# Kernel optimization log

Hardware: AMD Instinct MI355X
Metric: run time of the kernel (lower is better)

The kernel has to match this reference:

```python
import jax, jax.numpy as jnp
import numpy as np

D = 1024  # inputSize = stateSize = hiddenSize

def _linear_params(key, fan_in, fan_out):
    k1, k2 = jax.random.split(key)
    lim = 1.0 / np.sqrt(fan_in)
    W = jax.random.uniform(k1, (fan_out, fan_in), jnp.float32, -lim, lim)
    b = jax.random.uniform(k2, (fan_out,), jnp.float32, -lim, lim)
    return W, b

def setup_inputs() -> dict:
    key = jax.random.key(0)
    ks = jax.random.split(key, 6)
    x = jax.random.normal(ks[0], (64, D, 200), dtype=jnp.float32)
    W_in, b_in = _linear_params(ks[1], D, D)      # l1_in
    W_hid, b_hid = _linear_params(ks[2], D, D)    # l1_hid
    W2, b2 = _linear_params(ks[3], D, D)          # l2
    W3, b3 = _linear_params(ks[4], D, D)          # l3
    W_out, b_out = _linear_params(ks[5], D, D)    # l_out
    etas = jnp.full((5,), 0.01, dtype=jnp.float32)
    return {"x": x, "W_in": W_in, "b_in": b_in, "W_hid": W_hid, "b_hid": b_hid,
            "W2": W2, "b2": b2, "W3": W3, "b3": b3,
            "W_out": W_out, "b_out": b_out, "etas": etas}

def reference(x, W_in, b_in, W_hid, b_hid, W2, b2, W3, b3, W_out, b_out, etas):
    B = x.shape[0]
    elu = jax.nn.elu

    def step(h0, x_t):  # x_t: [B, D]
        wx = x_t @ W_in.T + b_in
        h = h0
        for k in range(5):  # five fixed-point iterations (eta1..eta5)
            u = (h + h0) @ W_hid.T + b_hid
            F1 = elu(u + wx)
            Fn = elu(elu(F1 @ W2.T + b2) @ W3.T + b3)
            h = h + etas[k] * (Fn - (h + h0))
        y = h @ W_out.T + b_out
        return h, y

    h0 = jnp.zeros((B, x.shape[1]), dtype=x.dtype)
    xs = jnp.transpose(x, (2, 0, 1))  # [T, B, D]
    _, ys = jax.lax.scan(step, h0, xs)  # ys: [T, B, D]
    return jnp.transpose(ys, (1, 2, 0))  # [B, D, T]
```

## Files before the change

### kernel.cpp

```cpp
#include <hip/hip_runtime.h>
#include <cmath>

#define DD 1024
#define TT 200
#define NWG 256
#define THR 512

__device__ __forceinline__ float eluf(float x) { return x > 0.f ? x : expm1f(x); }

__global__ __launch_bounds__(256) void transpose_k(const float* __restrict__ src,
                                                   float* __restrict__ dst) {
  __shared__ float tile[32][33];
  const int bx = blockIdx.x << 5;
  const int by = blockIdx.y << 5;
  const int tx = threadIdx.x & 31;
  const int ty = threadIdx.x >> 5;
#pragma unroll
  for (int i = 0; i < 4; ++i) {
    int r = ty + (i << 3);
    tile[r][tx] = src[(size_t)(bx + r) * DD + by + tx];
  }
  __syncthreads();
#pragma unroll
  for (int i = 0; i < 4; ++i) {
    int r = ty + (i << 3);
    dst[(size_t)(by + r) * DD + bx + tx] = tile[tx][r];
  }
}

__global__ __launch_bounds__(256) void wx_kernel(const float* __restrict__ x,
                                                 const float* __restrict__ Win,
                                                 const float* __restrict__ bin,
                                                 float* __restrict__ wxT) {
  const int gw = (blockIdx.x << 2) | (threadIdx.x >> 6);
  const int lane = threadIdx.x & 63;
  const int noct = gw & 127;
  const int tt = (gw >> 7) & 3;
  const int b = gw >> 9;
  const int n0 = noct << 3;
  const int t = (tt << 6) + lane;
  const int tl = t < TT ? t : (TT - 1);
  const float* xp = x + (size_t)b * DD * TT + tl;
  float acc[8];
#pragma unroll
  for (int j = 0; j < 8; ++j) acc[j] = 0.f;
  for (int k = 0; k < DD; k += 4) {
    float x0 = xp[(size_t)(k + 0) * TT];
    float x1 = xp[(size_t)(k + 1) * TT];
    float x2 = xp[(size_t)(k + 2) * TT];
    float x3 = xp[(size_t)(k + 3) * TT];
#pragma unroll
    for (int j = 0; j < 8; ++j) {
      const float4 w = *(const float4*)(Win + (size_t)(n0 + j) * DD + k);
      acc[j] = fmaf(x0, w.x, fmaf(x1, w.y, fmaf(x2, w.z, fmaf(x3, w.w, acc[j]))));
    }
  }
  if (t < TT) {
#pragma unroll
    for (int j = 0; j < 8; ++j)
      wxT[((size_t)b * DD + n0 + j) * TT + t] = acc[j] + bin[n0 + j];
  }
}

__device__ __forceinline__ float stage_gemm(const float* __restrict__ Wt,
                                            const float* __restrict__ inrows,
                                            float* __restrict__ in_s,
                                            float* __restrict__ red,
                                            int tid, int k0, int nn, int bg) {
  {
    const float4* __restrict__ s4 = (const float4*)inrows;
    float4* d4 = (float4*)in_s;
    float4 t0 = s4[tid], t1 = s4[tid + 512], t2 = s4[tid + 1024], t3 = s4[tid + 1536];
    d4[tid] = t0;
    d4[tid + 512] = t1;
    d4[tid + 1024] = t2;
    d4[tid + 1536] = t3;
  }
  __syncthreads();

  const float* wp = Wt + (size_t)k0 * DD + nn;
  const float* isp = in_s + ((bg << 2) << 10) + k0;
  float acc[4];
#pragma unroll
  for (int j = 0; j < 4; ++j) acc[j] = 0.f;
  float wa[8], wb[8];
#pragma unroll
  for (int j = 0; j < 8; ++j) wa[j] = wp[j * DD];

#pragma unroll
  for (int kk = 0; kk < 128; kk += 16) {
#pragma unroll
    for (int j = 0; j < 8; ++j) wb[j] = wp[(kk + 8 + j) * DD];
#pragma unroll
    for (int rr = 0; rr < 4; ++rr) {
      const float4 a = *(const float4*)(isp + (rr << 10) + kk);
      const float4 b = *(const float4*)(isp + (rr << 10) + kk + 4);
      acc[rr] = fmaf(a.x, wa[0], fmaf(a.y, wa[1], fmaf(a.z, wa[2], fmaf(a.w, wa[3], acc[rr]))));
      acc[rr] = fmaf(b.x, wa[4], fmaf(b.y, wa[5], fmaf(b.z, wa[6], fmaf(b.w, wa[7], acc[rr]))));
    }
#pragma unroll
    for (int j = 0; j < 8; ++j) wa[j] = wp[((kk + 16 + j) & 127) * DD];
#pragma unroll
    for (int rr = 0; rr < 4; ++rr) {
      const float4 a = *(const float4*)(isp + (rr << 10) + kk + 8);
      const float4 b = *(const float4*)(isp + (rr << 10) + kk + 12);
      acc[rr] = fmaf(a.x, wb[0], fmaf(a.y, wb[1], fmaf(a.z, wb[2], fmaf(a.w, wb[3], acc[rr]))));
      acc[rr] = fmaf(b.x, wb[4], fmaf(b.y, wb[5], fmaf(b.z, wb[6], fmaf(b.w, wb[7], acc[rr]))));
    }
  }

  const int ob = ((tid >> 6) << 8) + (bg << 7) + (nn & 31);
  red[ob] = acc[0];
  red[ob + 32] = acc[1];
  red[ob + 64] = acc[2];
  red[ob + 96] = acc[3];
  __syncthreads();
  float v = 0.f;
  if (tid < 256) {
#pragma unroll
    for (int w = 0; w < 8; ++w) v += red[(w << 8) + tid];
  }
  return v;
}

#define STAGE_PROLOGUE                                        \
  __shared__ float in_s[8192];                                \
  __shared__ float red[2048];                                 \
  const int tid = threadIdx.x;                                \
  const int lane = tid & 63;                                  \
  const int ntile = blockIdx.x & 31;                          \
  const int btile = blockIdx.x >> 5;                          \
  const int n0 = ntile << 5;                                  \
  const int b0 = btile << 3;                                  \
  const int nn = n0 + (lane & 31);                            \
  const int bg = lane >> 5;                                   \
  const int k0 = (tid >> 6) << 7;                             \
  const bool owner = tid < 256;                               \
  const int orow = (tid & 255) >> 5;                          \
  const int ocol = tid & 31;                                  \
  const size_t o = (size_t)(b0 + orow) * DD + (n0 + ocol);

__global__ void __launch_bounds__(THR, 1) kA(const float* __restrict__ WtH,
                                             const float* __restrict__ sbuf,
                                             const float* __restrict__ bh_,
                                             const float* __restrict__ wxT,
                                             float* __restrict__ F1b, int t) {
  STAGE_PROLOGUE
  float v = stage_gemm(WtH, sbuf + (size_t)b0 * DD, in_s, red, tid, k0, nn, bg);
  if (owner) F1b[o] = eluf(v + bh_[n0 + ocol] + wxT[o * TT + t]);
}

__global__ void __launch_bounds__(THR, 1) kB(const float* __restrict__ Wt2,
                                             const float* __restrict__ F1b,
                                             const float* __restrict__ b2_,
                                             float* __restrict__ Gb) {
  STAGE_PROLOGUE
  float v = stage_gemm(Wt2, F1b + (size_t)b0 * DD, in_s, red, tid, k0, nn, bg);
  if (owner) Gb[o] = eluf(v + b2_[n0 + ocol]);
}

__global__ void __launch_bounds__(THR, 1) kC(const float* __restrict__ Wt3,
                                             const float* __restrict__ Gb,
                                             const float* __restrict__ b3_,
                                             const float* __restrict__ etas_,
                                             float* __restrict__ h_cur,
                                             float* __restrict__ h0b,
                                             float* __restrict__ sbuf, int it) {
  STAGE_PROLOGUE
  float v = stage_gemm(Wt3, Gb + (size_t)b0 * DD, in_s, red, tid, k0, nn, bg);
  if (owner) {
    const float fn = eluf(v + b3_[n0 + ocol]);
    const float e = etas_[it];
    const float h = h_cur[o];
    const float h0 = h0b[o];
    const float hn = h + e * (fn - h - h0);
    h_cur[o] = hn;
    if (it == 4) {
      sbuf[o] = 2.f * hn;
      h0b[o] = hn;
    } else {
      sbuf[o] = hn + h0;
    }
  }
}

__global__ void __launch_bounds__(THR, 1) kO(const float* __restrict__ WtO,
                                             const float* __restrict__ h0b,
                                             const float* __restrict__ bo_,
                                             float* __restrict__ outp, int t) {
  STAGE_PROLOGUE
  float v = stage_gemm(WtO, h0b + (size_t)b0 * DD, in_s, red, tid, k0, nn, bg);
  if (owner) outp[o * TT + t] = v + bo_[n0 + ocol];
}

extern "C" void kernel_launch(void* const* d_in, const int* in_sizes, int n_in,
                              void* d_out, int out_size, void* d_ws, size_t ws_size,
                              hipStream_t stream) {
  const float* x = (const float*)d_in[0];
  const float* Win = (const float*)d_in[1];
  const float* bin = (const float*)d_in[2];
  const float* Whid = (const float*)d_in[3];
  const float* bhid = (const float*)d_in[4];
  const float* W2 = (const float*)d_in[5];
  const float* b2 = (const float*)d_in[6];
  const float* W3 = (const float*)d_in[7];
  const float* b3 = (const float*)d_in[8];
  const float* Wout = (const float*)d_in[9];
  const float* bout = (const float*)d_in[10];
  const float* etas = (const float*)d_in[11];
  float* out = (float*)d_out;

  char* ws = (char*)d_ws;
  float* wxT = (float*)(ws);
  float* WtH = (float*)(ws + 52428800);
  float* Wt2 = (float*)(ws + 56623104);
  float* Wt3 = (float*)(ws + 60817408);
  float* WtO = (float*)(ws + 65011712);
  float* sbuf = (float*)(ws + 69206016);
  float* F1b = (float*)(ws + 69468160);
  float* Gb = (float*)(ws + 69730304);
  float* h_cur = (float*)(ws + 69992448);
  float* h0b = (float*)(ws + 70254592);

  hipMemsetAsync(sbuf, 0, 262144, stream);
  hipMemsetAsync(h_cur, 0, 262144, stream);
  hipMemsetAsync(h0b, 0, 262144, stream);

  dim3 tb(256);
  dim3 tg(32, 32);
  hipLaunchKernelGGL(transpose_k, tg, tb, 0, stream, Whid, WtH);
  hipLaunchKernelGGL(transpose_k, tg, tb, 0, stream, W2, Wt2);
  hipLaunchKernelGGL(transpose_k, tg, tb, 0, stream, W3, Wt3);
  hipLaunchKernelGGL(transpose_k, tg, tb, 0, stream, Wout, WtO);
  hipLaunchKernelGGL(wx_kernel, dim3(8192), tb, 0, stream, x, Win, bin, wxT);

  const dim3 sg(NWG);
  const dim3 sb(THR);
  for (int t = 0; t < TT; ++t) {
    for (int it = 0; it < 5; ++it) {
      hipLaunchKernelGGL(kA, sg, sb, 0, stream, WtH, sbuf, bhid, wxT, F1b, t);
      hipLaunchKernelGGL(kB, sg, sb, 0, stream, Wt2, F1b, b2, Gb);
      hipLaunchKernelGGL(kC, sg, sb, 0, stream, Wt3, Gb, b3, etas, h_cur, h0b, sbuf, it);
    }
    hipLaunchKernelGGL(kO, sg, sb, 0, stream, WtO, h0b, bout, out, t);
  }
}
```

Baseline: 23.43 ms.

## Defer output projection to one batched launch and widen weight prefetch

Each timestep's final hidden state is stored to a workspace buffer when it fits, and all 200 output projections run after the recurrence in a single kOall launch with a 2D grid, replacing 200 serial kO launches inside the loop. The inner GEMM now preloads 16 weight rows per buffer instead of 8 and starts the first weight loads before the shared-memory barrier, to hide more global load latency. This needs about 52MB of extra workspace and falls back to the per-step path when that is not available. Register use rises with the larger weight buffers.

```diff
diff --git a/kernel.cpp b/kernel.cpp
--- a/kernel.cpp
+++ b/kernel.cpp
@@ -67,10 +67,14 @@
                                             float* __restrict__ in_s,
                                             float* __restrict__ red,
                                             int tid, int k0, int nn, int bg) {
+  const float* wp = Wt + (size_t)k0 * DD + nn;
+  float wa[16], wb[16];
   {
     const float4* __restrict__ s4 = (const float4*)inrows;
     float4* d4 = (float4*)in_s;
     float4 t0 = s4[tid], t1 = s4[tid + 512], t2 = s4[tid + 1024], t3 = s4[tid + 1536];
+#pragma unroll
+    for (int j = 0; j < 16; ++j) wa[j] = wp[j * DD];
     d4[tid] = t0;
     d4[tid + 512] = t1;
     d4[tid + 1024] = t2;
@@ -78,34 +82,40 @@
   }
   __syncthreads();
 
-  const float* wp = Wt + (size_t)k0 * DD + nn;
   const float* isp = in_s + ((bg << 2) << 10) + k0;
   float acc[4];
 #pragma unroll
   for (int j = 0; j < 4; ++j) acc[j] = 0.f;
-  float wa[8], wb[8];
-#pragma unroll
-  for (int j = 0; j < 8; ++j) wa[j] = wp[j * DD];
-
-#pragma unroll
-  for (int kk = 0; kk < 128; kk += 16) {
-#pragma unroll
-    for (int j = 0; j < 8; ++j) wb[j] = wp[(kk + 8 + j) * DD];
+
+#pragma unroll
+  for (int kk = 0; kk < 128; kk += 32) {
+#pragma unroll
+    for (int j = 0; j < 16; ++j) wb[j] = wp[(kk + 16 + j) * DD];
 #pragma unroll
     for (int rr = 0; rr < 4; ++rr) {
-      const float4 a = *(const float4*)(isp + (rr << 10) + kk);
-      const float4 b = *(const float4*)(isp + (rr << 10) + kk + 4);
+      const float* ip = isp + (rr << 10) + kk;
+      const float4 a = *(const float4*)(ip);
+      const float4 b = *(const float4*)(ip + 4);
+      const float4 c = *(const float4*)(ip + 8);
+      const float4 d = *(const float4*)(ip + 12);
       acc[rr] = fmaf(a.x, wa[0], fmaf(a.y, wa[1], fmaf(a.z, wa[2], fmaf(a.w, wa[3], acc[rr]))));
       acc[rr] = fmaf(b.x, wa[4], fmaf(b.y, wa[5], fmaf(b.z, wa[6], fmaf(b.w, wa[7], acc[rr]))));
-    }
-#pragma unroll
-    for (int j = 0; j < 8; ++j) wa[j] = wp[((kk + 16 + j) & 127) * DD];
+      acc[rr] = fmaf(c.x, wa[8], fmaf(c.y, wa[9], fmaf(c.z, wa[10], fmaf(c.w, wa[11], acc[rr]))));
+      acc[rr] = fmaf(d.x, wa[12], fmaf(d.y, wa[13], fmaf(d.z, wa[14], fmaf(d.w, wa[15], acc[rr]))));
+    }
+#pragma unroll
+    for (int j = 0; j < 16; ++j) wa[j] = wp[((kk + 32 + j) & 127) * DD];
 #pragma unroll
     for (int rr = 0; rr < 4; ++rr) {
-      const float4 a = *(const float4*)(isp + (rr << 10) + kk + 8);
-      const float4 b = *(const float4*)(isp + (rr << 10) + kk + 12);
+      const float* ip = isp + (rr << 10) + kk + 16;
+      const float4 a = *(const float4*)(ip);
+      const float4 b = *(const float4*)(ip + 4);
+      const float4 c = *(const float4*)(ip + 8);
+      const float4 d = *(const float4*)(ip + 12);
       acc[rr] = fmaf(a.x, wb[0], fmaf(a.y, wb[1], fmaf(a.z, wb[2], fmaf(a.w, wb[3], acc[rr]))));
       acc[rr] = fmaf(b.x, wb[4], fmaf(b.y, wb[5], fmaf(b.z, wb[6], fmaf(b.w, wb[7], acc[rr]))));
+      acc[rr] = fmaf(c.x, wb[8], fmaf(c.y, wb[9], fmaf(c.z, wb[10], fmaf(c.w, wb[11], acc[rr]))));
+      acc[rr] = fmaf(d.x, wb[12], fmaf(d.y, wb[13], fmaf(d.z, wb[14], fmaf(d.w, wb[15], acc[rr]))));
     }
   }
 
@@ -165,7 +175,9 @@
                                              const float* __restrict__ etas_,
                                              float* __restrict__ h_cur,
                                              float* __restrict__ h0b,
-                                             float* __restrict__ sbuf, int it) {
+                                             float* __restrict__ sbuf,
+                                             float* __restrict__ hall,
+                                             int it, int t) {
   STAGE_PROLOGUE
   float v = stage_gemm(Wt3, Gb + (size_t)b0 * DD, in_s, red, tid, k0, nn, bg);
   if (owner) {
@@ -178,6 +190,7 @@
     if (it == 4) {
       sbuf[o] = 2.f * hn;
       h0b[o] = hn;
+      if (hall) hall[(size_t)t * 65536 + o] = hn;
     } else {
       sbuf[o] = hn + h0;
     }
@@ -190,6 +203,17 @@
                                              float* __restrict__ outp, int t) {
   STAGE_PROLOGUE
   float v = stage_gemm(WtO, h0b + (size_t)b0 * DD, in_s, red, tid, k0, nn, bg);
+  if (owner) outp[o * TT + t] = v + bo_[n0 + ocol];
+}
+
+__global__ void __launch_bounds__(THR, 1) kOall(const float* __restrict__ WtO,
+                                                const float* __restrict__ hall,
+                                                const float* __restrict__ bo_,
+                                                float* __restrict__ outp) {
+  STAGE_PROLOGUE
+  const int t = blockIdx.y;
+  float v = stage_gemm(WtO, hall + (size_t)t * 65536 + (size_t)b0 * DD,
+                       in_s, red, tid, k0, nn, bg);
   if (owner) outp[o * TT + t] = v + bo_[n0 + ocol];
 }
 
@@ -221,6 +245,8 @@
   float* Gb = (float*)(ws + 69730304);
   float* h_cur = (float*)(ws + 69992448);
   float* h0b = (float*)(ws + 70254592);
+  const bool deferO = ws_size >= (70516736ull + 52428800ull);
+  float* hall = deferO ? (float*)(ws + 70516736) : nullptr;
 
   hipMemsetAsync(sbuf, 0, 262144, stream);
   hipMemsetAsync(h_cur, 0, 262144, stream);
@@ -240,8 +266,12 @@
     for (int it = 0; it < 5; ++it) {
       hipLaunchKernelGGL(kA, sg, sb, 0, stream, WtH, sbuf, bhid, wxT, F1b, t);
       hipLaunchKernelGGL(kB, sg, sb, 0, stream, Wt2, F1b, b2, Gb);
-      hipLaunchKernelGGL(kC, sg, sb, 0, stream, Wt3, Gb, b3, etas, h_cur, h0b, sbuf, it);
-    }
-    hipLaunchKernelGGL(kO, sg, sb, 0, stream, WtO, h0b, bout, out, t);
-  }
-}
+      hipLaunchKernelGGL(kC, sg, sb, 0, stream, Wt3, Gb, b3, etas, h_cur, h0b,
+                         sbuf, hall, it, t);
+    }
+    if (!deferO)
+      hipLaunchKernelGGL(kO, sg, sb, 0, stream, WtO, h0b, bout, out, t);
+  }
+  if (deferO)
+    hipLaunchKernelGGL(kOall, dim3(NWG, TT), sb, 0, stream, WtO, hall, bout, out);
+}
```

New measurement: 23.06 ms. About the same (-1.5%).
